# Kernel tuning notes

Measured on AMD Instinct MI355X. Metric: run time of the kernel, lower is better.

## Reference

```python
import jax, jax.numpy as jnp
import numpy as np
import math

D_MODEL = 1024
D_INNER = 2048
D_HALF = D_INNER // 2
D_STATE = 16
D_CONV = 4
DT_RANK = 64
B_SZ = 4
L = 2048


def _dw_conv(x, w, b):
    # x: (b, l, c), w: (k, 1, c) depthwise, SAME padding
    y = jax.lax.conv_general_dilated(
        x, w, window_strides=(1,), padding='SAME',
        feature_group_count=x.shape[-1],
        dimension_numbers=('NWC', 'WIO', 'NWC'))
    return y + b


def _selective_scan(u, delta, A, Bc, Cc, D):
    # u, delta: (b, l, d); Bc, Cc: (b, l, n); A: (d, n); D: (d,)
    b, l, d = u.shape
    n = A.shape[1]

    def step(h, inp):
        d_t, u_t, B_t, C_t = inp  # (b,d), (b,d), (b,n), (b,n)
        dA = jnp.exp(d_t[..., None] * A)                     # (b,d,n)
        h = dA * h + (d_t * u_t)[..., None] * B_t[:, None, :]
        y = jnp.einsum('bdn,bn->bd', h, C_t)
        return h, y

    h0 = jnp.zeros((b, d, n), u.dtype)
    xs = (jnp.moveaxis(delta, 1, 0), jnp.moveaxis(u, 1, 0),
          jnp.moveaxis(Bc, 1, 0), jnp.moveaxis(Cc, 1, 0))
    _, ys = jax.lax.scan(step, h0, xs)                       # (l,b,d)
    return jnp.moveaxis(ys, 0, 1) + u * D


def setup_inputs() -> dict:
    key = jax.random.key(0)
    ks = jax.random.split(key, 12)
    x = jax.random.normal(ks[0], (B_SZ, L, D_MODEL), jnp.float32)
    W_in = jax.random.normal(ks[1], (D_MODEL, D_INNER), jnp.float32) * (D_MODEL ** -0.5)
    conv_x_w = jax.random.normal(ks[2], (D_CONV, 1, D_HALF), jnp.float32) * (D_CONV ** -0.5)
    conv_x_b = jnp.zeros((D_HALF,), jnp.float32)
    conv_z_w = jax.random.normal(ks[3], (D_CONV, 1, D_HALF), jnp.float32) * (D_CONV ** -0.5)
    conv_z_b = jnp.zeros((D_HALF,), jnp.float32)
    W_xdbl = jax.random.normal(ks[4], (D_HALF, DT_RANK + 2 * D_STATE), jnp.float32) * (D_HALF ** -0.5)
    dt_init_std = DT_RANK ** -0.5  # dt_scale = 1.0
    W_dt = jax.random.uniform(ks[5], (DT_RANK, D_HALF), jnp.float32, -dt_init_std, dt_init_std)
    rand_vals = jax.random.uniform(ks[6], (D_HALF,))
    dt_bias = jnp.exp(rand_vals * (math.log(0.1) - math.log(0.001)) + math.log(0.001))
    dt_bias = jnp.clip(dt_bias, 1e-4)
    inv_dt = dt_bias + jnp.log(-jnp.expm1(-dt_bias))
    D = jnp.ones((D_HALF,), jnp.float32)
    W_out = jax.random.normal(ks[7], (D_INNER, D_MODEL), jnp.float32) * (D_INNER ** -0.5)
    b_out = jnp.zeros((D_MODEL,), jnp.float32)
    return dict(x=x, W_in=W_in, conv_x_w=conv_x_w, conv_x_b=conv_x_b,
                conv_z_w=conv_z_w, conv_z_b=conv_z_b, W_xdbl=W_xdbl,
                W_dt=W_dt, inv_dt=inv_dt, D=D, W_out=W_out, b_out=b_out)


def reference(x, W_in, conv_x_w, conv_x_b, conv_z_w, conv_z_b, W_xdbl,
              W_dt, inv_dt, D, W_out, b_out):
    xz = x @ W_in                                            # (b,l,d_inner), no bias
    xs, z = jnp.split(xz, 2, axis=-1)                        # (b,l,d_half) each
    # A = -exp(log(arange(1..N))) tiled over channels
    A = -jnp.tile(jnp.arange(1, D_STATE + 1, dtype=jnp.float32), (D_HALF, 1))  # (d,n)
    xs = jax.nn.silu(_dw_conv(xs, conv_x_w, conv_x_b))
    z = jax.nn.silu(_dw_conv(z, conv_z_w, conv_z_b))
    x_dbl = xs @ W_xdbl                                      # (b,l,dt_rank+2n)
    dt_low, Bc, Cc = jnp.split(x_dbl, [DT_RANK, DT_RANK + D_STATE], axis=-1)
    dt = dt_low @ W_dt + inv_dt                              # Dense with bias_init=inv_dt
    delta = jax.nn.softplus(dt + inv_dt)                     # scan adds delta_bias=inv_dt again (faithful)
    y = _selective_scan(xs, delta, A, Bc, Cc, D)             # (b,l,d_half)
    y = jnp.concatenate([y, z], axis=-1)                     # (b,l,d_inner)
    return y @ W_out + b_out
```

## Files before the change

### kernel.cpp

```cpp
#include <hip/hip_runtime.h>
#include <hip/hip_bf16.h>
#include <math.h>

#define B_SZ 4
#define LSEQ 2048
#define DM 1024
#define DI 2048
#define DH 1024
#define DS 16
#define DTR 64
#define RTOT 96
#define MROWS (B_SZ * LSEQ)

#define NCH 32
#define CHUNK 64

typedef short bf8_t __attribute__((ext_vector_type(8)));
typedef float f4_t __attribute__((ext_vector_type(4)));

__device__ __forceinline__ unsigned short f2bfbits(float v) {
  __hip_bfloat16 h = __float2bfloat16(v);
  return *(unsigned short*)&h;
}
__device__ __forceinline__ float bfu_lo(unsigned int v) {
  unsigned int x = v << 16;
  return *(float*)&x;
}
__device__ __forceinline__ float bfu_hi(unsigned int v) {
  unsigned int x = v & 0xffff0000u;
  return *(float*)&x;
}

__device__ __forceinline__ void gl_lds16(const void* g, void* l) {
  __builtin_amdgcn_global_load_lds(
      (const __attribute__((address_space(1))) unsigned int*)g,
      (__attribute__((address_space(3))) unsigned int*)l,
      16, 0, 0);
}

__device__ __forceinline__ void ld8f(const float* p, unsigned short* d) {
  const float4 a = ((const float4*)p)[0];
  const float4 b = ((const float4*)p)[1];
  d[0] = f2bfbits(a.x); d[1] = f2bfbits(a.y); d[2] = f2bfbits(a.z); d[3] = f2bfbits(a.w);
  d[4] = f2bfbits(b.x); d[5] = f2bfbits(b.y); d[6] = f2bfbits(b.z); d[7] = f2bfbits(b.w);
}

__global__ void probe_kernel(const unsigned short* __restrict__ p, int* __restrict__ flag) {
  int lane = threadIdx.x;
  int sane = 0;
#pragma unroll
  for (int j = 0; j < 4; j++) {
    unsigned short lo = p[(lane * 4 + j) * 2];
    int e = (lo >> 7) & 0xFF;
    sane += (e <= 130) ? 1 : 0;
  }
  sane += __shfl_xor(sane, 1, 64);
  sane += __shfl_xor(sane, 2, 64);
  sane += __shfl_xor(sane, 4, 64);
  sane += __shfl_xor(sane, 8, 64);
  sane += __shfl_xor(sane, 16, 64);
  sane += __shfl_xor(sane, 32, 64);
  if (lane == 0) *flag = (sane >= 220) ? 1 : 0;
}

#define PREP_TOT 78848
__global__ __launch_bounds__(256) void prep_kernel(
    const int* __restrict__ flag,
    const void* s0, const void* s1, const void* s2, const void* s3,
    const void* s4, const void* s5, const void* s6, const void* s7,
    float* __restrict__ out) {
  int i = blockIdx.x * 256 + threadIdx.x;
  if (i >= PREP_TOT) return;
  const void* src; int off;
  if      (i < 4096)   { src = s0; off = i; }
  else if (i < 5120)   { src = s1; off = i - 4096; }
  else if (i < 9216)   { src = s2; off = i - 5120; }
  else if (i < 10240)  { src = s3; off = i - 9216; }
  else if (i < 75776)  { src = s4; off = i - 10240; }
  else if (i < 76800)  { src = s5; off = i - 75776; }
  else if (i < 77824)  { src = s6; off = i - 76800; }
  else                 { src = s7; off = i - 77824; }
  float v = (*flag == 1) ? __bfloat162float(((const __hip_bfloat16*)src)[off])
                         : ((const float*)src)[off];
  out[i] = v;
}

__global__ __launch_bounds__(256) void transpose_kernel(
    const int* __restrict__ flag, const void* __restrict__ W,
    unsigned short* __restrict__ Wt, int K, int N) {
  __shared__ unsigned short tile[32][33];
  int n0 = blockIdx.x * 32, k0 = blockIdx.y * 32;
  int c = threadIdx.x & 31, r8 = threadIdx.x >> 5;
  bool isbf = (*flag == 1);
#pragma unroll
  for (int p = 0; p < 4; p++) {
    int r = r8 + p * 8;
    unsigned short v;
    if (isbf) v = ((const unsigned short*)W)[(size_t)(k0 + r) * N + n0 + c];
    else      v = f2bfbits(((const float*)W)[(size_t)(k0 + r) * N + n0 + c]);
    tile[r][c] = v;
  }
  __syncthreads();
#pragma unroll
  for (int p = 0; p < 4; p++) {
    int r = r8 + p * 8;
    Wt[(size_t)(n0 + r) * K + k0 + c] = tile[c][r];
  }
}

__global__ __launch_bounds__(256) void transpose_pad_kernel(
    const int* __restrict__ flag, const void* __restrict__ W,
    unsigned short* __restrict__ Wt) {
  __shared__ unsigned short tile[32][33];
  int n0 = blockIdx.x * 32, k0 = blockIdx.y * 32;
  int c = threadIdx.x & 31, r8 = threadIdx.x >> 5;
  bool isbf = (*flag == 1);
#pragma unroll
  for (int p = 0; p < 4; p++) {
    int r = r8 + p * 8;
    unsigned short v = 0;
    if (n0 + c < RTOT) {
      if (isbf) v = ((const unsigned short*)W)[(size_t)(k0 + r) * RTOT + n0 + c];
      else      v = f2bfbits(((const float*)W)[(size_t)(k0 + r) * RTOT + n0 + c]);
    }
    tile[r][c] = v;
  }
  __syncthreads();
#pragma unroll
  for (int p = 0; p < 4; p++) {
    int r = r8 + p * 8;
    Wt[(size_t)(n0 + r) * DH + k0 + c] = tile[c][r];
  }
}

template <bool A_BF, bool O_BF>
__global__ __launch_bounds__(256) void gemm_tpl(
    const int* __restrict__ flag, int want,
    const void* __restrict__ A, const unsigned short* __restrict__ Bt,
    const float* __restrict__ bias, void* __restrict__ C,
    int M, int N, int K) {
  if (*flag != want) return;
  __shared__ __align__(16) unsigned short As[128 * 64];
  __shared__ __align__(16) unsigned short Bs[128 * 64];
  const int tid = threadIdx.x;
  const int lane = tid & 63;
  const int wave = tid >> 6;
  const int quad = lane >> 4;
  const int l16 = lane & 15;
  const int wm = (wave & 1) * 64;
  const int wn = (wave >> 1) * 64;

  const int NB = gridDim.x, MB = gridDim.y;
  int L = blockIdx.y * NB + blockIdx.x;
  int xcd = L & 7;
  int w = L >> 3;
  int m_band = xcd * (MB >> 3) + (w / NB);
  int n_blk = w % NB;
  const int m0 = m_band * 128;
  const int n0 = n_blk * 128;

  f4_t acc[4][4] = {};

  for (int k0 = 0; k0 < K; k0 += 64) {
#pragma unroll
    for (int j = 0; j < 4; j++) {
      int ch = tid + j * 256;
      int mi = ch >> 3;
      int s = ch & 7;
      int ki = (s & 4) | ((s & 3) ^ ((mi >> 1) & 3));
      if (A_BF) {
        gl_lds16((const unsigned short*)A + (size_t)(m0 + mi) * K + k0 + ki * 8,
                 &As[(j * 256 + wave * 64) * 8]);
      } else {
        unsigned short tmp[8];
        ld8f((const float*)A + (size_t)(m0 + mi) * K + k0 + ki * 8, tmp);
        *(uint4*)&As[ch * 8] = *(uint4*)tmp;
      }
    }
#pragma unroll
    for (int j = 0; j < 4; j++) {
      int ch = tid + j * 256;
      int ni = ch >> 3;
      int s = ch & 7;
      int ki = (s & 4) | ((s & 3) ^ ((ni >> 1) & 3));
      gl_lds16(Bt + (size_t)(n0 + ni) * K + k0 + ki * 8,
               &Bs[(j * 256 + wave * 64) * 8]);
    }
    __syncthreads();

#pragma unroll
    for (int h = 0; h < 2; h++) {
      bf8_t af[4], bfr[4];
#pragma unroll
      for (int ti = 0; ti < 4; ti++) {
        int r = wm + ti * 16 + l16;
        af[ti] = *(const bf8_t*)&As[(r * 8 + h * 4 + (quad ^ ((r >> 1) & 3))) * 8];
      }
#pragma unroll
      for (int tj = 0; tj < 4; tj++) {
        int r = wn + tj * 16 + l16;
        bfr[tj] = *(const bf8_t*)&Bs[(r * 8 + h * 4 + (quad ^ ((r >> 1) & 3))) * 8];
      }
#pragma unroll
      for (int ti = 0; ti < 4; ti++)
#pragma unroll
        for (int tj = 0; tj < 4; tj++)
          acc[ti][tj] = __builtin_amdgcn_mfma_f32_16x16x32_bf16(
              af[ti], bfr[tj], acc[ti][tj], 0, 0, 0);
    }
    __syncthreads();
  }

#pragma unroll
  for (int ti = 0; ti < 4; ti++) {
#pragma unroll
    for (int tj = 0; tj < 4; tj++) {
      int col = n0 + wn + tj * 16 + l16;
      float bv = bias ? bias[col] : 0.f;
#pragma unroll
      for (int r = 0; r < 4; r++) {
        int row = m0 + wm + ti * 16 + quad * 4 + r;
        float v = acc[ti][tj][r] + bv;
        if (O_BF) ((__hip_bfloat16*)C)[(size_t)row * N + col] = __float2bfloat16(v);
        else      ((float*)C)[(size_t)row * N + col] = v;
      }
    }
  }
}

__global__ __launch_bounds__(256) void xdbl_mfma_kernel(
    const unsigned short* __restrict__ A, const unsigned short* __restrict__ Bt,
    float* __restrict__ xdbl) {
  __shared__ __align__(16) unsigned short As[64 * 32];
  __shared__ __align__(16) unsigned short Bs[128 * 32];
  const int tid = threadIdx.x;
  const int lane = tid & 63;
  const int wave = tid >> 6;
  const int quad = lane >> 4;
  const int l16 = lane & 15;
  const int m0 = blockIdx.x * 64;

  f4_t acc[6] = {};

  for (int k0 = 0; k0 < DH; k0 += 32) {
    {
      int ch = tid;
      int mi = ch >> 2;
      int ki = (ch & 3) ^ ((mi >> 1) & 3);
      gl_lds16(A + (size_t)(m0 + mi) * DH + k0 + ki * 8, &As[(wave * 64) * 8]);
    }
#pragma unroll
    for (int j = 0; j < 2; j++) {
      int ch = tid + j * 256;
      int ni = ch >> 2;
      int ki = (ch & 3) ^ ((ni >> 1) & 3);
      gl_lds16(Bt + (size_t)ni * DH + k0 + ki * 8, &Bs[(j * 256 + wave * 64) * 8]);
    }
    __syncthreads();

    bf8_t af, bfr[6];
    {
      int r = wave * 16 + l16;
      af = *(const bf8_t*)&As[(r * 4 + (quad ^ ((r >> 1) & 3))) * 8];
    }
#pragma unroll
    for (int tj = 0; tj < 6; tj++) {
      int r = tj * 16 + l16;
      bfr[tj] = *(const bf8_t*)&Bs[(r * 4 + (quad ^ ((r >> 1) & 3))) * 8];
    }
#pragma unroll
    for (int tj = 0; tj < 6; tj++)
      acc[tj] = __builtin_amdgcn_mfma_f32_16x16x32_bf16(af, bfr[tj], acc[tj], 0, 0, 0);
    __syncthreads();
  }

#pragma unroll
  for (int tj = 0; tj < 6; tj++) {
    int col = tj * 16 + l16;
#pragma unroll
    for (int r = 0; r < 4; r++) {
      int row = m0 + wave * 16 + quad * 4 + r;
      xdbl[(size_t)row * RTOT + col] = acc[tj][r];
    }
  }
}

__global__ __launch_bounds__(256) void conv_silu_kernel(
    const unsigned short* __restrict__ xz,
    const float* __restrict__ wx, const float* __restrict__ bx,
    const float* __restrict__ wz, const float* __restrict__ bz,
    unsigned short* __restrict__ xs_bf, unsigned short* __restrict__ cat) {
  int gid = blockIdx.x * 256 + threadIdx.x;
  int cg = gid & 127;
  int c0 = cg * 8;
  int m = gid >> 7;
  int t = m & (LSEQ - 1);
  float ax[8], az[8];
#pragma unroll
  for (int i = 0; i < 8; i++) { ax[i] = bx[c0 + i]; az[i] = bz[c0 + i]; }
#pragma unroll
  for (int j = 0; j < 4; j++) {
    int tt = t - 1 + j;
    if (tt < 0 || tt >= LSEQ) continue;
    size_t row = (size_t)(m - t + tt);
    uint4 vx = *(const uint4*)&xz[row * DI + c0];
    uint4 vz = *(const uint4*)&xz[row * DI + DH + c0];
    const unsigned int* px = (const unsigned int*)&vx;
    const unsigned int* pz = (const unsigned int*)&vz;
#pragma unroll
    for (int q = 0; q < 4; q++) {
      float x0 = bfu_lo(px[q]), x1 = bfu_hi(px[q]);
      float z0 = bfu_lo(pz[q]), z1 = bfu_hi(pz[q]);
      ax[q * 2]     = fmaf(wx[j * DH + c0 + q * 2], x0, ax[q * 2]);
      ax[q * 2 + 1] = fmaf(wx[j * DH + c0 + q * 2 + 1], x1, ax[q * 2 + 1]);
      az[q * 2]     = fmaf(wz[j * DH + c0 + q * 2], z0, az[q * 2]);
      az[q * 2 + 1] = fmaf(wz[j * DH + c0 + q * 2 + 1], z1, az[q * 2 + 1]);
    }
  }
  unsigned short sx[8], sz[8];
#pragma unroll
  for (int i = 0; i < 8; i++) {
    float vx = ax[i] / (1.f + __expf(-ax[i]));
    float vz = az[i] / (1.f + __expf(-az[i]));
    sx[i] = f2bfbits(vx);
    sz[i] = f2bfbits(vz);
  }
  *(uint4*)&xs_bf[(size_t)m * DH + c0] = *(uint4*)sx;
  *(uint4*)&cat[(size_t)m * DI + DH + c0] = *(uint4*)sz;
}

__global__ __launch_bounds__(256) void delta_kernel(
    const float* __restrict__ xdbl, const float* __restrict__ Wdt,
    const float* __restrict__ inv_dt, const unsigned short* __restrict__ xs,
    unsigned int* __restrict__ du) {
  const int d = blockIdx.x * 256 + threadIdx.x;
  const int m0 = blockIdx.y * 8;
  __shared__ float xr[8][DTR];
#pragma unroll
  for (int i = 0; i < 2; i++) {
    int e = threadIdx.x + i * 256;
    xr[e >> 6][e & 63] = xdbl[(size_t)(m0 + (e >> 6)) * RTOT + (e & 63)];
  }
  __syncthreads();
  float acc[8];
#pragma unroll
  for (int i = 0; i < 8; i++) acc[i] = 0.f;
  for (int rr = 0; rr < DTR; rr++) {
    float w = Wdt[(size_t)rr * DH + d];
#pragma unroll
    for (int i = 0; i < 8; i++) acc[i] = fmaf(xr[i][rr], w, acc[i]);
  }
  const float bias2 = 2.f * inv_dt[d];
#pragma unroll
  for (int i = 0; i < 8; i++) {
    float v = acc[i] + bias2;
    float sp = (v > 0.f) ? (v + log1pf(__expf(-v))) : log1pf(__expf(v));
    unsigned int lo = f2bfbits(sp);
    unsigned int hi = xs[(size_t)(m0 + i) * DH + d];
    du[(size_t)(m0 + i) * DH + d] = lo | (hi << 16);
  }
}

__global__ __launch_bounds__(256) void scan_pass1(
    const unsigned int* __restrict__ du, const float* __restrict__ xdbl,
    float* __restrict__ Echunks, float* __restrict__ hp) {
  const int tid = threadIdx.x;
  const int d = blockIdx.x * 256 + tid;
  const int c = blockIdx.y, b = blockIdx.z;
  const int row0 = b * LSEQ + c * CHUNK;
  __shared__ float sBC[CHUNK][32];
#pragma unroll
  for (int i = 0; i < 2; i++) {
    int task = tid + i * 256;
    int r = task >> 3, seg = task & 7;
    *(float4*)&sBC[r][seg * 4] =
        *(const float4*)&xdbl[(size_t)(row0 + r) * RTOT + DTR + seg * 4];
  }
  __syncthreads();
  float h[16];
#pragma unroll
  for (int n = 0; n < 16; n++) h[n] = 0.f;
  float E = 1.f;
  for (int t = 0; t < CHUNK; t++) {
    unsigned int v = du[(size_t)(row0 + t) * DH + d];
    float dt = bfu_lo(v), ut = bfu_hi(v);
    float e = __expf(-dt);
    E *= e;
    float dv = dt * ut;
    float p = 1.f;
#pragma unroll
    for (int n = 0; n < 16; n++) {
      p *= e;
      h[n] = fmaf(p, h[n], dv * sBC[t][n]);
    }
  }
  Echunks[((size_t)c * B_SZ + b) * DH + d] = E;
#pragma unroll
  for (int n = 0; n < 16; n++)
    hp[(((size_t)c * B_SZ + b) * 16 + n) * DH + d] = h[n];
}

__global__ __launch_bounds__(256) void scan_pass2(
    const float* __restrict__ Echunks, const float* __restrict__ hp,
    float* __restrict__ hs) {
  int t = blockIdx.x * 256 + threadIdx.x;
  int d = t & 1023;
  int n = (t >> 10) & 15;
  int b = t >> 14;
  float h = 0.f;
  const int k0 = n + 1;
  for (int c = 0; c < NCH; c++) {
    float E = Echunks[((size_t)c * B_SZ + b) * DH + d];
    float a = 1.f, base = E;
    int k = k0;
#pragma unroll
    for (int i = 0; i < 5; i++) {
      if (k & 1) a *= base;
      base *= base;
      k >>= 1;
    }
    size_t idx = (((size_t)c * B_SZ + b) * 16 + n) * DH + d;
    hs[idx] = h;
    h = fmaf(a, h, hp[idx]);
  }
}

__global__ __launch_bounds__(256) void scan_pass3(
    const unsigned int* __restrict__ du, const float* __restrict__ xdbl,
    const float* __restrict__ hs, const float* __restrict__ Dvec,
    __hip_bfloat16* __restrict__ cat) {
  const int tid = threadIdx.x;
  const int d = blockIdx.x * 256 + tid;
  const int c = blockIdx.y, b = blockIdx.z;
  const int row0 = b * LSEQ + c * CHUNK;
  __shared__ float sBC[CHUNK][32];
#pragma unroll
  for (int i = 0; i < 2; i++) {
    int task = tid + i * 256;
    int r = task >> 3, seg = task & 7;
    *(float4*)&sBC[r][seg * 4] =
        *(const float4*)&xdbl[(size_t)(row0 + r) * RTOT + DTR + seg * 4];
  }
  __syncthreads();
  float h[16];
#pragma unroll
  for (int n = 0; n < 16; n++)
    h[n] = hs[(((size_t)c * B_SZ + b) * 16 + n) * DH + d];
  const float Dd = Dvec[d];
  for (int t = 0; t < CHUNK; t++) {
    unsigned int v = du[(size_t)(row0 + t) * DH + d];
    float dt = bfu_lo(v), ut = bfu_hi(v);
    float e = __expf(-dt);
    float dv = dt * ut;
    float p = 1.f, y = 0.f;
#pragma unroll
    for (int n = 0; n < 16; n++) {
      p *= e;
      h[n] = fmaf(p, h[n], dv * sBC[t][n]);
      y = fmaf(h[n], sBC[t][16 + n], y);
    }
    y = fmaf(ut, Dd, y);
    cat[(size_t)(row0 + t) * DI + d] = __float2bfloat16(y);
  }
}

extern "C" void kernel_launch(void* const* d_in, const int* in_sizes, int n_in,
                              void* d_out, int out_size, void* d_ws, size_t ws_size,
                              hipStream_t stream) {
  char* ws = (char*)d_ws;
  __hip_bfloat16* xz  = (__hip_bfloat16*)(ws);
  unsigned int* du    = (unsigned int*)(ws);
  __hip_bfloat16* xs  = (__hip_bfloat16*)(ws + ((size_t)32 << 20));
  __hip_bfloat16* cat = (__hip_bfloat16*)(ws + ((size_t)64 << 20));
  float* xdbl         = (float*)(ws + ((size_t)96 << 20));
  float* Echunks      = (float*)(ws + ((size_t)99 << 20));
  float* hp           = (float*)(ws + ((size_t)100 << 20));
  float* hs           = (float*)(ws + ((size_t)108 << 20));
  unsigned short* Wt_in  = (unsigned short*)(ws + ((size_t)116 << 20));
  unsigned short* Wt_out = (unsigned short*)(ws + ((size_t)120 << 20));
  unsigned short* Wxt    = (unsigned short*)(ws + ((size_t)124 << 20));
  float* cw           = (float*)(ws + ((size_t)125 << 20));
  int* flag           = (int*)(ws + ((size_t)126 << 20));

  const float* conv_xwf = cw + 0;
  const float* conv_xbf = cw + 4096;
  const float* conv_zwf = cw + 5120;
  const float* conv_zbf = cw + 9216;
  const float* Wdtf     = cw + 10240;
  const float* inv_dtf  = cw + 75776;
  const float* Df       = cw + 76800;
  const float* b_outf   = cw + 77824;

  probe_kernel<<<1, 64, 0, stream>>>((const unsigned short*)d_in[0], flag);
  prep_kernel<<<(PREP_TOT + 255) / 256, 256, 0, stream>>>(
      flag, d_in[2], d_in[3], d_in[4], d_in[5], d_in[7], d_in[8], d_in[9],
      d_in[11], cw);
  transpose_kernel<<<dim3(DI / 32, DM / 32), 256, 0, stream>>>(
      flag, d_in[1], Wt_in, DM, DI);
  transpose_kernel<<<dim3(DM / 32, DI / 32), 256, 0, stream>>>(
      flag, d_in[10], Wt_out, DI, DM);
  transpose_pad_kernel<<<dim3(4, DH / 32), 256, 0, stream>>>(flag, d_in[6], Wxt);

  gemm_tpl<true, true><<<dim3(DI / 128, MROWS / 128), 256, 0, stream>>>(
      flag, 1, d_in[0], Wt_in, (const float*)nullptr, xz, MROWS, DI, DM);
  gemm_tpl<false, true><<<dim3(DI / 128, MROWS / 128), 256, 0, stream>>>(
      flag, 0, d_in[0], Wt_in, (const float*)nullptr, xz, MROWS, DI, DM);
  conv_silu_kernel<<<(MROWS * 128) / 256, 256, 0, stream>>>(
      (const unsigned short*)xz, conv_xwf, conv_xbf, conv_zwf, conv_zbf,
      (unsigned short*)xs, (unsigned short*)cat);
  xdbl_mfma_kernel<<<MROWS / 64, 256, 0, stream>>>(
      (const unsigned short*)xs, Wxt, xdbl);
  delta_kernel<<<dim3(4, MROWS / 8), 256, 0, stream>>>(
      xdbl, Wdtf, inv_dtf, (const unsigned short*)xs, du);
  scan_pass1<<<dim3(4, NCH, B_SZ), 256, 0, stream>>>(du, xdbl, Echunks, hp);
  scan_pass2<<<256, 256, 0, stream>>>(Echunks, hp, hs);
  scan_pass3<<<dim3(4, NCH, B_SZ), 256, 0, stream>>>(du, xdbl, hs, Df, cat);
  gemm_tpl<true, true><<<dim3(DM / 128, MROWS / 128), 256, 0, stream>>>(
      flag, 1, cat, Wt_out, b_outf, d_out, MROWS, DM, DI);
  gemm_tpl<true, false><<<dim3(DM / 128, MROWS / 128), 256, 0, stream>>>(
      flag, 0, cat, Wt_out, b_outf, d_out, MROWS, DM, DI);
}
```

Measured before the change: 383.0 us.

## Use 256-row double-buffered GEMM tiles with 512 threads and new LDS swizzle

Replaces the 128x128 single-buffered GEMM with a 256xBN tile (BN=256 for the input projection, 128 for the output projection) computed by 512 threads. The next K-slice is loaded into a second LDS buffer while the current one feeds the MFMAs, with a full 8-way XOR swizzle and s_setprio raised around the MFMA block. This aims for more operand reuse per byte loaded and to hide global-to-LDS latency. The cost is large dynamic LDS (up to 128KB), more accumulator registers, and fewer blocks in flight: the 8192x2048 GEMM drops from 1024 to 256 blocks, which may underfill 256 CUs. Inside the loop there is only one barrier, placed after the MFMAs, so correctness depends on async gl_lds writes being visible before the next iteration reads them.

```diff
diff --git a/kernel.cpp b/kernel.cpp
--- a/kernel.cpp
+++ b/kernel.cpp
@@ -133,22 +133,25 @@
   }
 }
 
-template <bool A_BF, bool O_BF>
-__global__ __launch_bounds__(256) void gemm_tpl(
+template <int BN, bool A_BF, bool O_BF>
+__global__ __launch_bounds__(512, 2) void gemm256_tpl(
     const int* __restrict__ flag, int want,
     const void* __restrict__ A, const unsigned short* __restrict__ Bt,
     const float* __restrict__ bias, void* __restrict__ C,
     int M, int N, int K) {
   if (*flag != want) return;
-  __shared__ __align__(16) unsigned short As[128 * 64];
-  __shared__ __align__(16) unsigned short Bs[128 * 64];
+  extern __shared__ __align__(16) unsigned short lds[];
+  constexpr int A_TILE = 256 * 64;
+  constexpr int B_TILE = BN * 64;
+  constexpr int NF = BN / 64;
+
   const int tid = threadIdx.x;
   const int lane = tid & 63;
   const int wave = tid >> 6;
   const int quad = lane >> 4;
   const int l16 = lane & 15;
-  const int wm = (wave & 1) * 64;
-  const int wn = (wave >> 1) * 64;
+  const int wm = wave >> 2;
+  const int wn = wave & 3;
 
   const int NB = gridDim.x, MB = gridDim.y;
   int L = blockIdx.y * NB + blockIdx.x;
@@ -156,70 +159,81 @@
   int w = L >> 3;
   int m_band = xcd * (MB >> 3) + (w / NB);
   int n_blk = w % NB;
-  const int m0 = m_band * 128;
-  const int n0 = n_blk * 128;
-
-  f4_t acc[4][4] = {};
-
-  for (int k0 = 0; k0 < K; k0 += 64) {
+  const int m0 = m_band * 256;
+  const int n0 = n_blk * BN;
+
+  f4_t acc[8][NF] = {};
+
+  auto stage = [&](int k0, int b) {
+    unsigned short* Ad = lds + b * A_TILE;
 #pragma unroll
     for (int j = 0; j < 4; j++) {
-      int ch = tid + j * 256;
-      int mi = ch >> 3;
-      int s = ch & 7;
-      int ki = (s & 4) | ((s & 3) ^ ((mi >> 1) & 3));
+      int ch = tid + j * 512;
+      int mi = ch >> 3, s = ch & 7;
+      int ki = s ^ (mi & 7);
       if (A_BF) {
         gl_lds16((const unsigned short*)A + (size_t)(m0 + mi) * K + k0 + ki * 8,
-                 &As[(j * 256 + wave * 64) * 8]);
+                 Ad + (j * 512 + wave * 64) * 8);
       } else {
         unsigned short tmp[8];
         ld8f((const float*)A + (size_t)(m0 + mi) * K + k0 + ki * 8, tmp);
-        *(uint4*)&As[ch * 8] = *(uint4*)tmp;
+        *(uint4*)&Ad[ch * 8] = *(uint4*)tmp;
       }
     }
-#pragma unroll
-    for (int j = 0; j < 4; j++) {
-      int ch = tid + j * 256;
-      int ni = ch >> 3;
-      int s = ch & 7;
-      int ki = (s & 4) | ((s & 3) ^ ((ni >> 1) & 3));
+    unsigned short* Bd = lds + 2 * A_TILE + b * B_TILE;
+#pragma unroll
+    for (int j = 0; j < NF; j++) {
+      int ch = tid + j * 512;
+      int ni = ch >> 3, s = ch & 7;
+      int ki = s ^ (ni & 7);
       gl_lds16(Bt + (size_t)(n0 + ni) * K + k0 + ki * 8,
-               &Bs[(j * 256 + wave * 64) * 8]);
-    }
-    __syncthreads();
-
+               Bd + (j * 512 + wave * 64) * 8);
+    }
+  };
+
+  stage(0, 0);
+  __syncthreads();
+  int cur = 0;
+  for (int k0 = 0; k0 < K; k0 += 64) {
+    if (k0 + 64 < K) stage(k0 + 64, cur ^ 1);
+
+    const unsigned short* Ac = lds + cur * A_TILE;
+    const unsigned short* Bc = lds + 2 * A_TILE + cur * B_TILE;
 #pragma unroll
     for (int h = 0; h < 2; h++) {
-      bf8_t af[4], bfr[4];
-#pragma unroll
-      for (int ti = 0; ti < 4; ti++) {
-        int r = wm + ti * 16 + l16;
-        af[ti] = *(const bf8_t*)&As[(r * 8 + h * 4 + (quad ^ ((r >> 1) & 3))) * 8];
+      bf8_t af[8], bfr[NF];
+#pragma unroll
+      for (int ti = 0; ti < 8; ti++) {
+        int r = wm * 128 + ti * 16 + l16;
+        af[ti] = *(const bf8_t*)&Ac[(r * 8 + ((h * 4 + quad) ^ (r & 7))) * 8];
       }
 #pragma unroll
-      for (int tj = 0; tj < 4; tj++) {
-        int r = wn + tj * 16 + l16;
-        bfr[tj] = *(const bf8_t*)&Bs[(r * 8 + h * 4 + (quad ^ ((r >> 1) & 3))) * 8];
+      for (int tj = 0; tj < NF; tj++) {
+        int rn = wn * (BN / 4) + tj * 16 + l16;
+        bfr[tj] = *(const bf8_t*)&Bc[(rn * 8 + ((h * 4 + quad) ^ (rn & 7))) * 8];
       }
-#pragma unroll
-      for (int ti = 0; ti < 4; ti++)
-#pragma unroll
-        for (int tj = 0; tj < 4; tj++)
+      __builtin_amdgcn_s_setprio(1);
+#pragma unroll
+      for (int ti = 0; ti < 8; ti++)
+#pragma unroll
+        for (int tj = 0; tj < NF; tj++)
           acc[ti][tj] = __builtin_amdgcn_mfma_f32_16x16x32_bf16(
               af[ti], bfr[tj], acc[ti][tj], 0, 0, 0);
+      __builtin_amdgcn_s_setprio(0);
     }
     __syncthreads();
-  }
-
-#pragma unroll
-  for (int ti = 0; ti < 4; ti++) {
-#pragma unroll
-    for (int tj = 0; tj < 4; tj++) {
-      int col = n0 + wn + tj * 16 + l16;
+    cur ^= 1;
+  }
+
+#pragma unroll
+  for (int ti = 0; ti < 8; ti++) {
+#pragma unroll
+    for (int tj = 0; tj < NF; tj++) {
+      int col = n0 + wn * (BN / 4) + tj * 16 + l16;
       float bv = bias ? bias[col] : 0.f;
 #pragma unroll
       for (int r = 0; r < 4; r++) {
-        int row = m0 + wm + ti * 16 + quad * 4 + r;
+        int row = m0 + wm * 128 + ti * 16 + quad * 4 + r;
         float v = acc[ti][tj][r] + bv;
         if (O_BF) ((__hip_bfloat16*)C)[(size_t)row * N + col] = __float2bfloat16(v);
         else      ((float*)C)[(size_t)row * N + col] = v;
@@ -491,6 +505,15 @@
   const float* Df       = cw + 76800;
   const float* b_outf   = cw + 77824;
 
+  (void)hipFuncSetAttribute(reinterpret_cast<const void*>(&gemm256_tpl<256, true, true>),
+                            hipFuncAttributeMaxDynamicSharedMemorySize, 131072);
+  (void)hipFuncSetAttribute(reinterpret_cast<const void*>(&gemm256_tpl<256, false, true>),
+                            hipFuncAttributeMaxDynamicSharedMemorySize, 131072);
+  (void)hipFuncSetAttribute(reinterpret_cast<const void*>(&gemm256_tpl<128, true, true>),
+                            hipFuncAttributeMaxDynamicSharedMemorySize, 98304);
+  (void)hipFuncSetAttribute(reinterpret_cast<const void*>(&gemm256_tpl<128, true, false>),
+                            hipFuncAttributeMaxDynamicSharedMemorySize, 98304);
+
   probe_kernel<<<1, 64, 0, stream>>>((const unsigned short*)d_in[0], flag);
   prep_kernel<<<(PREP_TOT + 255) / 256, 256, 0, stream>>>(
       flag, d_in[2], d_in[3], d_in[4], d_in[5], d_in[7], d_in[8], d_in[9],
@@ -501,9 +524,9 @@
       flag, d_in[10], Wt_out, DI, DM);
   transpose_pad_kernel<<<dim3(4, DH / 32), 256, 0, stream>>>(flag, d_in[6], Wxt);
 
-  gemm_tpl<true, true><<<dim3(DI / 128, MROWS / 128), 256, 0, stream>>>(
+  gemm256_tpl<256, true, true><<<dim3(DI / 256, MROWS / 256), 512, 131072, stream>>>(
       flag, 1, d_in[0], Wt_in, (const float*)nullptr, xz, MROWS, DI, DM);
-  gemm_tpl<false, true><<<dim3(DI / 128, MROWS / 128), 256, 0, stream>>>(
+  gemm256_tpl<256, false, true><<<dim3(DI / 256, MROWS / 256), 512, 131072, stream>>>(
       flag, 0, d_in[0], Wt_in, (const float*)nullptr, xz, MROWS, DI, DM);
   conv_silu_kernel<<<(MROWS * 128) / 256, 256, 0, stream>>>(
       (const unsigned short*)xz, conv_xwf, conv_xbf, conv_zwf, conv_zbf,
@@ -515,8 +538,8 @@
   scan_pass1<<<dim3(4, NCH, B_SZ), 256, 0, stream>>>(du, xdbl, Echunks, hp);
   scan_pass2<<<256, 256, 0, stream>>>(Echunks, hp, hs);
   scan_pass3<<<dim3(4, NCH, B_SZ), 256, 0, stream>>>(du, xdbl, hs, Df, cat);
-  gemm_tpl<true, true><<<dim3(DM / 128, MROWS / 128), 256, 0, stream>>>(
+  gemm256_tpl<128, true, true><<<dim3(DM / 128, MROWS / 256), 512, 98304, stream>>>(
       flag, 1, cat, Wt_out, b_outf, d_out, MROWS, DM, DI);
-  gemm_tpl<true, false><<<dim3(DM / 128, MROWS / 128), 256, 0, stream>>>(
+  gemm256_tpl<128, true, false><<<dim3(DM / 128, MROWS / 256), 512, 98304, stream>>>(
       flag, 0, cat, Wt_out, b_outf, d_out, MROWS, DM, DI);
 }
```

New measurement: 373.5 us. -2.5%, faster.
